# Kernel tuning notes

Hardware: AMD Instinct MI355X
Metric: run time of the kernel (lower is better)

Reference implementation:

```python
import jax, jax.numpy as jnp
import numpy as np

WS = 16            # window size (patch grid)
NP = WS * WS       # 256 patch tokens
N = NP + 1         # +1 CLS
H = 16             # heads
LN_EPS = 1e-5


def _rel_pos_index():
    ch, cw = np.meshgrid(np.arange(WS), np.arange(WS), indexing='ij')
    flat = np.stack([ch.reshape(-1), cw.reshape(-1)])            # [2, NP]
    rel = flat[:, :, None] - flat[:, None, :]                    # [2, NP, NP]
    rel = rel.transpose(1, 2, 0).astype(np.int64)                # [NP, NP, 2]
    rel[:, :, 0] += WS - 1
    rel[:, :, 1] += WS - 1
    rel[:, :, 0] *= 2 * WS - 1
    nrd = (2 * WS - 1) * (2 * WS - 1) + 3                        # 964
    idx = np.zeros((N, N), dtype=np.int64)
    idx[1:, 1:] = rel.sum(-1)
    idx[0, 0:] = nrd - 3
    idx[0:, 0] = nrd - 2
    idx[0, 0] = nrd - 1
    return idx

REL_IDX = _rel_pos_index()


def layernorm(x, g, b):
    mu = x.mean(-1, keepdims=True)
    var = x.var(-1, keepdims=True)
    return (x - mu) * jax.lax.rsqrt(var + LN_EPS) * g + b


def rotate_half(t):
    t1, t2 = t[..., ::2], t[..., 1::2]
    return jnp.stack([-t2, t1], axis=-1).reshape(t.shape)


def apply_rope(t, cos, sin):
    # t: [B, H, NP, hd]; cos/sin: [NP, hd]
    return t * cos + rotate_half(t) * sin


def setup_inputs() -> dict:
    key = jax.random.key(0)
    ks = jax.random.split(key, 20)
    D, Hd = 1024, 4096
    s = lambda d: 1.0 / np.sqrt(d)
    return {
        'x': jax.random.normal(ks[0], (64, N, D), jnp.float32),
        'rope_cos': jnp.cos(jnp.arange(NP)[:, None] * jnp.exp(-jnp.arange(64) / 16.0)[None, :]),
        'rope_sin': jnp.sin(jnp.arange(NP)[:, None] * jnp.exp(-jnp.arange(64) / 16.0)[None, :]),
        'q_w': jax.random.normal(ks[1], (D, D)) * s(D),
        'q_b': jnp.zeros((D,)),
        'k_w': jax.random.normal(ks[2], (D, D)) * s(D),
        'v_w': jax.random.normal(ks[3], (D, D)) * s(D),
        'v_b': jnp.zeros((D,)),
        'rel_bias_table': jax.random.normal(ks[4], (964, H)) * 0.02,
        'inner_ln_g': jnp.ones((D,)), 'inner_ln_b': jnp.zeros((D,)),
        'proj_w': jax.random.normal(ks[5], (D, D)) * s(D),
        'proj_b': jnp.zeros((D,)),
        'norm1_g': jnp.ones((D,)), 'norm1_b': jnp.zeros((D,)),
        'norm2_g': jnp.ones((D,)), 'norm2_b': jnp.zeros((D,)),
        'w1_w': jax.random.normal(ks[6], (Hd, D)) * s(D),
        'w1_b': jnp.zeros((Hd,)),
        'w2_w': jax.random.normal(ks[7], (Hd, D)) * s(D),
        'w2_b': jnp.zeros((Hd,)),
        'ffn_ln_g': jnp.ones((Hd,)), 'ffn_ln_b': jnp.zeros((Hd,)),
        'w3_w': jax.random.normal(ks[8], (D, Hd)) * s(Hd),
        'w3_b': jnp.zeros((D,)),
    }


def reference(x, rope_cos, rope_sin, q_w, q_b, k_w, v_w, v_b, rel_bias_table,
              inner_ln_g, inner_ln_b, proj_w, proj_b, norm1_g, norm1_b,
              norm2_g, norm2_b, w1_w, w1_b, w2_w, w2_b, ffn_ln_g, ffn_ln_b,
              w3_w, w3_b):
    B, Ntok, D = x.shape
    hd = D // H
    scale = hd ** -0.5

    # ---- attention branch (pre-norm, subln path) ----
    xn = layernorm(x, norm1_g, norm1_b)
    q = (xn @ q_w.T + q_b).reshape(B, Ntok, H, hd).transpose(0, 2, 1, 3)
    k = (xn @ k_w.T).reshape(B, Ntok, H, hd).transpose(0, 2, 1, 3)
    v = (xn @ v_w.T + v_b).reshape(B, Ntok, H, hd).transpose(0, 2, 1, 3)

    # RoPE on all tokens except CLS
    q = jnp.concatenate([q[:, :, :1], apply_rope(q[:, :, 1:], rope_cos, rope_sin)], axis=2)
    k = jnp.concatenate([k[:, :, :1], apply_rope(k[:, :, 1:], rope_cos, rope_sin)], axis=2)

    attn = jnp.einsum('bhqd,bhkd->bhqk', q * scale, k)
    # relative position bias: [N, N, H] -> [H, N, N]
    rel_bias = rel_bias_table[REL_IDX.reshape(-1)].reshape(Ntok, Ntok, H).transpose(2, 0, 1)
    attn = attn + rel_bias[None]
    attn = jax.nn.softmax(attn, axis=-1)

    out = jnp.einsum('bhqk,bhkd->bqhd', attn, v).reshape(B, Ntok, D)
    out = layernorm(out, inner_ln_g, inner_ln_b)     # inner_attn_ln (subln)
    out = out @ proj_w.T + proj_b
    x = x + out

    # ---- SwiGLU MLP branch ----
    xn2 = layernorm(x, norm2_g, norm2_b)
    x1 = xn2 @ w1_w.T + w1_b
    x2 = xn2 @ w2_w.T + w2_b
    hidden = jax.nn.silu(x1) * x2
    hidden = layernorm(hidden, ffn_ln_g, ffn_ln_b)   # ffn_ln (subln)
    x = x + (hidden @ w3_w.T + w3_b)
    return x
```

## Files before the change

kernel.cpp:

```cpp
#include <hip/hip_runtime.h>
#include <stdint.h>

typedef __bf16 bf16;
typedef __attribute__((ext_vector_type(8))) __bf16 bf16x8;
typedef __attribute__((ext_vector_type(4))) float floatx4;

__device__ inline float bflo(uint32_t u){ union{uint32_t v; float f;} t; t.v = u << 16; return t.f; }
__device__ inline float bfhi(uint32_t u){ union{uint32_t v; float f;} t; t.v = u & 0xffff0000u; return t.f; }
__device__ inline uint32_t pack2(float a, float b){ union{ bf16 h[2]; uint32_t u; } t; t.h[0]=(bf16)a; t.h[1]=(bf16)b; return t.u; }

__device__ inline void load4(const bf16* p, float* x){
  uint2 u = *(const uint2*)p; x[0]=bflo(u.x); x[1]=bfhi(u.x); x[2]=bflo(u.y); x[3]=bfhi(u.y);
}
__device__ inline void load4(const float* p, float* x){
  float4 u = *(const float4*)p; x[0]=u.x; x[1]=u.y; x[2]=u.z; x[3]=u.w;
}

__device__ inline void gload16(const void* g, void* l){
  __builtin_amdgcn_global_load_lds((const __attribute__((address_space(1))) uint32_t*)g,
                                   (__attribute__((address_space(3))) uint32_t*)l, 16, 0, 0);
}

__global__ __launch_bounds__(256) void cvt_kernel(const float* __restrict__ in, bf16* __restrict__ out,
                                                  int n8, float scale)
{
  int i = blockIdx.x * 256 + threadIdx.x;
  if (i >= n8) return;
  const float* p = in + (size_t)i * 8;
  float4 a = *(const float4*)p;
  float4 b = *(const float4*)(p + 4);
  union{ uint4 q; bf16 h[8]; } pk;
  pk.h[0]=(bf16)(a.x*scale); pk.h[1]=(bf16)(a.y*scale); pk.h[2]=(bf16)(a.z*scale); pk.h[3]=(bf16)(a.w*scale);
  pk.h[4]=(bf16)(b.x*scale); pk.h[5]=(bf16)(b.y*scale); pk.h[6]=(bf16)(b.z*scale); pk.h[7]=(bf16)(b.w*scale);
  *(uint4*)(out + (size_t)i*8) = pk.q;
}

__global__ __launch_bounds__(256) void qkvb_fill(const float* __restrict__ qb, const float* __restrict__ vb,
                                                 float* __restrict__ out)
{
  int i = blockIdx.x * 256 + threadIdx.x;
  float v = 0.f;
  if (i < 1024) v = qb[i] * 0.125f;
  else if (i >= 2048) v = vb[i - 2048];
  out[i] = v;
}

__global__ __launch_bounds__(256) void bias_fill(const float* __restrict__ tab, bf16* __restrict__ biasB)
{
  int t = blockIdx.x * 256 + threadIdx.x;
  if (t >= 16*272*272) return;
  int kg = t % 272;
  int rem = t / 272;
  int qg = rem % 272;
  int h = rem / 272;
  float v;
  if (kg > 256) v = -3e38f;
  else {
    int qq = min(qg, 256);
    int idx;
    if (qq == 0 && kg == 0) idx = 963;
    else if (qq == 0) idx = 961;
    else if (kg == 0) idx = 962;
    else { int p = qq - 1, pk = kg - 1;
           idx = ((p >> 4) - (pk >> 4) + 15) * 31 + ((p & 15) - (pk & 15) + 15); }
    v = tab[idx*16 + h];
  }
  biasB[t] = (bf16)v;
}

template<int W, typename TIN>
__global__ __launch_bounds__(256) void ln_kernel(const TIN* in, const float* __restrict__ g,
                                                 const float* __restrict__ bb, bf16* out, int M)
{
  constexpr int E = W / 256;
  int row = blockIdx.x; if (row >= M) return;
  int tid = threadIdx.x;
  const TIN* rp = in + (size_t)row * W + tid * E;
  float x[E];
  #pragma unroll
  for (int j = 0; j < E; j += 4) load4(rp + j, &x[j]);
  float s = 0.f, ss = 0.f;
  #pragma unroll
  for (int e = 0; e < E; e++){ s += x[e]; ss += x[e]*x[e]; }
  #pragma unroll
  for (int k = 32; k >= 1; k >>= 1){ s += __shfl_xor(s, k, 64); ss += __shfl_xor(ss, k, 64); }
  __shared__ float rs_[4], rq_[4];
  if ((tid & 63) == 0){ rs_[tid >> 6] = s; rq_[tid >> 6] = ss; }
  __syncthreads();
  s = rs_[0]+rs_[1]+rs_[2]+rs_[3]; ss = rq_[0]+rq_[1]+rq_[2]+rq_[3];
  float mean = s * (1.0f / W);
  float var  = ss * (1.0f / W) - mean * mean;
  float rinv = rsqrtf(var + 1e-5f);
  bf16* op = out + (size_t)row * W + tid * E;
  const float* gp = g + tid * E;
  const float* bp = bb + tid * E;
  #pragma unroll
  for (int j = 0; j < E; j += 4){
    float gv[4], bv[4];
    load4(gp + j, gv); load4(bp + j, bv);
    float y0 = (x[j]  -mean)*rinv*gv[0] + bv[0];
    float y1 = (x[j+1]-mean)*rinv*gv[1] + bv[1];
    float y2 = (x[j+2]-mean)*rinv*gv[2] + bv[2];
    float y3 = (x[j+3]-mean)*rinv*gv[3] + bv[3];
    uint2 o; o.x = pack2(y0, y1); o.y = pack2(y2, y3);
    *(uint2*)(op + j) = o;
  }
}

template<typename TE, typename TC>
__global__ __launch_bounds__(256) void gemm_bt(const bf16* __restrict__ A, const bf16* __restrict__ Bw,
                                               const float* __restrict__ bias, const TE* extra,
                                               TC* C, int M, int N, int K, int mode)
{
  __shared__ __align__(16) bf16 As[128*32];
  __shared__ __align__(16) bf16 Bs[128*32];
  int tid = threadIdx.x;
  int lane = tid & 63, wave = tid >> 6;
  int l16 = lane & 15, quad = lane >> 4;
  int wm = wave >> 1, wn = wave & 1;
  int m0 = blockIdx.y * 128, n0 = blockIdx.x * 128;
  floatx4 acc[4][4];
  #pragma unroll
  for (int i = 0; i < 4; i++)
    #pragma unroll
    for (int j = 0; j < 4; j++) acc[i][j] = (floatx4){0.f,0.f,0.f,0.f};
  int nk = K >> 5;
  int rowS = tid >> 2;
  int colS = (tid & 3) * 8;
  int ra0 = min(m0 + rowS,      M-1);
  int ra1 = min(m0 + 64 + rowS, M-1);
  int rb0 = min(n0 + rowS,      N-1);
  int rb1 = min(n0 + 64 + rowS, N-1);
  const bf16* pa0 = A  + (size_t)ra0 * K + colS;
  const bf16* pa1 = A  + (size_t)ra1 * K + colS;
  const bf16* pb0 = Bw + (size_t)rb0 * K + colS;
  const bf16* pb1 = Bw + (size_t)rb1 * K + colS;
  bf16* la0 = &As[tid*8];        bf16* la1 = &As[2048 + tid*8];
  bf16* lb0 = &Bs[tid*8];        bf16* lb1 = &Bs[2048 + tid*8];
  auto stage = [&](int kt){
    int ko = kt * 32;
    gload16(pa0 + ko, la0);
    gload16(pa1 + ko, la1);
    gload16(pb0 + ko, lb0);
    gload16(pb1 + ko, lb1);
  };
  stage(0);
  int kt = 0;
  while (true){
    __syncthreads();
    bf16x8 af[4], bfv[4];
    #pragma unroll
    for (int i = 0; i < 4; i++) af[i]  = *(const bf16x8*)&As[(wm*64 + i*16 + l16)*32 + quad*8];
    #pragma unroll
    for (int j = 0; j < 4; j++) bfv[j] = *(const bf16x8*)&Bs[(wn*64 + j*16 + l16)*32 + quad*8];
    ++kt;
    bool more = kt < nk;
    if (more){
      __syncthreads();
      stage(kt);
    }
    #pragma unroll
    for (int i = 0; i < 4; i++)
      #pragma unroll
      for (int j = 0; j < 4; j++)
        acc[i][j] = __builtin_amdgcn_mfma_f32_16x16x32_bf16(af[i], bfv[j], acc[i][j], 0, 0, 0);
    if (!more) break;
  }
  #pragma unroll
  for (int i = 0; i < 4; i++){
    int gmb = m0 + wm*64 + i*16 + quad*4;
    #pragma unroll
    for (int j = 0; j < 4; j++){
      int gn = n0 + wn*64 + j*16 + l16;
      float bv = bias ? bias[gn] : 0.f;
      #pragma unroll
      for (int r = 0; r < 4; r++){
        int gm = gmb + r;
        if (gm < M){
          float v = acc[i][j][r] + bv;
          if (mode == 1) v += (float)extra[(size_t)gm * N + gn];
          else if (mode == 2){ float a = (float)extra[(size_t)gm * N + gn]; v *= a / (1.f + __expf(-a)); }
          C[(size_t)gm * N + gn] = (TC)v;
        }
      }
    }
  }
}

__global__ __launch_bounds__(256) void rope_kernel(bf16* __restrict__ qkv,
                                                   const float* __restrict__ cs, const float* __restrict__ sn)
{
  uint32_t i = blockIdx.x * 256u + threadIdx.x;
  int d0 = (int)(i & 511) * 2;
  int tok = (int)((i >> 9) & 255);
  int b = (int)(i >> 17);
  int j = d0 & 63;
  float c0 = cs[tok*64 + j], c1 = cs[tok*64 + j + 1];
  float s0 = sn[tok*64 + j], s1 = sn[tok*64 + j + 1];
  size_t off = ((size_t)(b*257 + tok + 1)) * 3072 + d0;
  uint32_t uq = *(const uint32_t*)(qkv + off);
  float x0 = bflo(uq), x1 = bfhi(uq);
  *(uint32_t*)(qkv + off) = pack2(x0*c0 - x1*s0, x1*c1 + x0*s1);
  uint32_t uk = *(const uint32_t*)(qkv + off + 1024);
  float y0 = bflo(uk), y1 = bfhi(uk);
  *(uint32_t*)(qkv + off + 1024) = pack2(y0*c0 - y1*s0, y1*c1 + y0*s1);
}

__global__ __launch_bounds__(256, 2) void attn_kernel(const bf16* __restrict__ QKV,
                                                      const bf16* __restrict__ biasB,
                                                      bf16* __restrict__ AO)
{
  __shared__ __align__(16) bf16 Ks[272*64];
  __shared__ __align__(16) bf16 Vt[64*296];
  int id = blockIdx.x;
  int h = id & 15, b = id >> 4;
  int tid = threadIdx.x, lane = tid & 63, wave = tid >> 6;
  int l16 = lane & 15, quad = lane >> 4;
  size_t baseQ = (size_t)(b*257) * 3072 + h*64;
  const bf16* Kg = QKV + baseQ + 1024;
  const bf16* Vg = QKV + baseQ + 2048;
  size_t aoBase = (size_t)(b*257) * 1024 + h*64;

  for (int i = tid; i < 272*8; i += 256){
    int row = i >> 3, seg = i & 7;
    int tok = min(row, 256);
    gload16(Kg + (size_t)tok*3072 + ((seg ^ (row & 7)) * 8), &Ks[i*8]);
  }
  for (int i = tid; i < 144*8; i += 256){
    int tp = (i % 144) * 2, dseg = i / 144;
    uint4 u0 = make_uint4(0,0,0,0), u1 = make_uint4(0,0,0,0);
    if (tp     <= 256) u0 = *(const uint4*)(Vg + (size_t)tp*3072 + dseg*8);
    if (tp + 1 <= 256) u1 = *(const uint4*)(Vg + (size_t)(tp+1)*3072 + dseg*8);
    union { uint4 q4; bf16 h8[8]; } va, vb2; va.q4 = u0; vb2.q4 = u1;
    #pragma unroll
    for (int jj = 0; jj < 8; jj++){
      union { uint32_t u; bf16 hh[2]; } w; w.hh[0] = va.h8[jj]; w.hh[1] = vb2.h8[jj];
      *(uint32_t*)&Vt[(dseg*8 + jj)*296 + tp] = w.u;
    }
  }
  __syncthreads();

  int srcA = l16 + 16*((2*quad)     & 3);
  int srcB = l16 + 16*((2*quad + 1) & 3);

  for (int qt = wave; qt < 17; qt += 4){
    int q0 = qt * 16;
    int qrow = min(q0 + l16, 256);
    const bf16* qp = QKV + baseQ + (size_t)qrow*3072;
    bf16x8 qb0 = *(const bf16x8*)(qp + quad*8);
    bf16x8 qb1 = *(const bf16x8*)(qp + 32 + quad*8);

    floatx4 S[17];
    #pragma unroll
    for (int nt = 0; nt < 17; nt++){
      int row = nt*16 + l16;
      bf16x8 ka0 = *(const bf16x8*)&Ks[row*64 + ((quad     ^ (l16 & 7)) * 8)];
      bf16x8 ka1 = *(const bf16x8*)&Ks[row*64 + (((4+quad) ^ (l16 & 7)) * 8)];
      floatx4 c = (floatx4){0.f,0.f,0.f,0.f};
      c = __builtin_amdgcn_mfma_f32_16x16x32_bf16(ka0, qb0, c, 0, 0, 0);
      c = __builtin_amdgcn_mfma_f32_16x16x32_bf16(ka1, qb1, c, 0, 0, 0);
      S[nt] = c;
    }

    const bf16* bp = biasB + ((size_t)(h*272) + (q0 + l16)) * 272;
    float m = -3e38f;
    #pragma unroll
    for (int nt = 0; nt < 17; nt++){
      uint2 bu = *(const uint2*)(bp + nt*16 + quad*4);
      S[nt][0] += bflo(bu.x); S[nt][1] += bfhi(bu.x);
      S[nt][2] += bflo(bu.y); S[nt][3] += bfhi(bu.y);
      m = fmaxf(m, fmaxf(fmaxf(S[nt][0], S[nt][1]), fmaxf(S[nt][2], S[nt][3])));
    }
    m = fmaxf(m, __shfl_xor(m, 16, 64));
    m = fmaxf(m, __shfl_xor(m, 32, 64));

    float lsum = 0.f;
    uint32_t pklo[17], pkhi[17];
    #pragma unroll
    for (int nt = 0; nt < 17; nt++){
      float p0 = __expf(S[nt][0] - m), p1 = __expf(S[nt][1] - m);
      float p2 = __expf(S[nt][2] - m), p3 = __expf(S[nt][3] - m);
      lsum += (p0 + p1) + (p2 + p3);
      pklo[nt] = pack2(p0, p1); pkhi[nt] = pack2(p2, p3);
    }
    lsum += __shfl_xor(lsum, 16, 64);
    lsum += __shfl_xor(lsum, 32, 64);

    floatx4 o[4];
    #pragma unroll
    for (int dt = 0; dt < 4; dt++) o[dt] = (floatx4){0.f,0.f,0.f,0.f};
    #pragma unroll
    for (int ks = 0; ks < 9; ks++){
      uint32_t t0[4], t1[4];
      t0[0] = (uint32_t)__shfl((int)pklo[2*ks], srcA, 64);
      t0[1] = (uint32_t)__shfl((int)pkhi[2*ks], srcA, 64);
      t0[2] = (uint32_t)__shfl((int)pklo[2*ks], srcB, 64);
      t0[3] = (uint32_t)__shfl((int)pkhi[2*ks], srcB, 64);
      if (2*ks + 1 <= 16){
        t1[0] = (uint32_t)__shfl((int)pklo[2*ks+1], srcA, 64);
        t1[1] = (uint32_t)__shfl((int)pkhi[2*ks+1], srcA, 64);
        t1[2] = (uint32_t)__shfl((int)pklo[2*ks+1], srcB, 64);
        t1[3] = (uint32_t)__shfl((int)pkhi[2*ks+1], srcB, 64);
      } else {
        t1[0] = 0; t1[1] = 0; t1[2] = 0; t1[3] = 0;
      }
      union { uint32_t u[4]; bf16x8 v; } pa;
      bool lowhalf = (quad < 2);
      pa.u[0] = lowhalf ? t0[0] : t1[0];
      pa.u[1] = lowhalf ? t0[1] : t1[1];
      pa.u[2] = lowhalf ? t0[2] : t1[2];
      pa.u[3] = lowhalf ? t0[3] : t1[3];
      #pragma unroll
      for (int dt = 0; dt < 4; dt++){
        bf16x8 vb = *(const bf16x8*)&Vt[(dt*16 + l16)*296 + ks*32 + quad*8];
        o[dt] = __builtin_amdgcn_mfma_f32_16x16x32_bf16(pa.v, vb, o[dt], 0, 0, 0);
      }
    }

    #pragma unroll
    for (int r = 0; r < 4; r++){
      int q = q0 + quad*4 + r;
      float ls = __shfl(lsum, quad*4 + r, 64);
      float rinv = 1.0f / ls;
      if (q <= 256){
        #pragma unroll
        for (int dt = 0; dt < 4; dt++)
          AO[aoBase + (size_t)q*1024 + dt*16 + l16] = (bf16)(o[dt][r] * rinv);
      }
    }
  }
}

extern "C" void kernel_launch(void* const* d_in, const int* in_sizes, int n_in,
                              void* d_out, int out_size, void* d_ws, size_t ws_size,
                              hipStream_t stream)
{
  (void)in_sizes; (void)n_in; (void)out_size; (void)ws_size;
  const float* x    = (const float*)d_in[0];
  const float* rc   = (const float*)d_in[1];
  const float* rsn  = (const float*)d_in[2];
  const float* q_w  = (const float*)d_in[3];
  const float* q_b  = (const float*)d_in[4];
  const float* k_w  = (const float*)d_in[5];
  const float* v_w  = (const float*)d_in[6];
  const float* v_b  = (const float*)d_in[7];
  const float* tab  = (const float*)d_in[8];
  const float* ig   = (const float*)d_in[9];
  const float* ib   = (const float*)d_in[10];
  const float* pw   = (const float*)d_in[11];
  const float* pb   = (const float*)d_in[12];
  const float* n1g  = (const float*)d_in[13];
  const float* n1b  = (const float*)d_in[14];
  const float* n2g  = (const float*)d_in[15];
  const float* n2b  = (const float*)d_in[16];
  const float* w1w  = (const float*)d_in[17];
  const float* w1b  = (const float*)d_in[18];
  const float* w2w  = (const float*)d_in[19];
  const float* w2b  = (const float*)d_in[20];
  const float* fg   = (const float*)d_in[21];
  const float* fb   = (const float*)d_in[22];
  const float* w3w  = (const float*)d_in[23];
  const float* w3b  = (const float*)d_in[24];

  const int M = 64 * 257;
  const int D = 1024, HD = 4096;
  char* ws = (char*)d_ws;
  const size_t CHB = (size_t)M * D * 2;
  bf16* B0 = (bf16*)(ws);
  bf16* B1 = (bf16*)(ws + CHB);
  bf16* B2 = (bf16*)(ws + 2*CHB);
  bf16* B3 = (bf16*)(ws + 3*CHB);
  bf16* WQ = (bf16*)(ws + 4*CHB);
  bf16* WK = WQ + (size_t)D*D;
  bf16* WV = WK + (size_t)D*D;
  bf16* WP = WV + (size_t)D*D;
  bf16* W1 = WP + (size_t)D*D;
  bf16* W2 = W1 + (size_t)HD*D;
  bf16* W3 = W2 + (size_t)HD*D;
  float* QKVB = (float*)(W3 + (size_t)HD*D);
  bf16* XN  = B0;
  bf16* QKV = B1;
  bf16* AO  = B0;
  bf16* AOL = B1;
  bf16* X1  = B2;
  bf16* XN2 = B3;
  bf16* HS  = B0;
  bf16* biasB = (bf16*)d_out;
  float* OUT = (float*)d_out;

  dim3 blk(256);
  dim3 g1(D/128, (M + 127)/128);
  dim3 gqkv(3072/128, (M + 127)/128);

  const int n8_D = D*D/8;
  const int n8_H = HD*D/8;
  cvt_kernel<<<dim3(n8_D/256), blk, 0, stream>>>(q_w, WQ, n8_D, 0.125f);
  cvt_kernel<<<dim3(n8_D/256), blk, 0, stream>>>(k_w, WK, n8_D, 1.f);
  cvt_kernel<<<dim3(n8_D/256), blk, 0, stream>>>(v_w, WV, n8_D, 1.f);
  cvt_kernel<<<dim3(n8_D/256), blk, 0, stream>>>(pw,  WP, n8_D, 1.f);
  cvt_kernel<<<dim3(n8_H/256), blk, 0, stream>>>(w1w, W1, n8_H, 1.f);
  cvt_kernel<<<dim3(n8_H/256), blk, 0, stream>>>(w2w, W2, n8_H, 1.f);
  cvt_kernel<<<dim3(n8_H/256), blk, 0, stream>>>(w3w, W3, n8_H, 1.f);
  qkvb_fill<<<dim3(12), blk, 0, stream>>>(q_b, v_b, QKVB);
  bias_fill<<<dim3((16*272*272 + 255)/256), blk, 0, stream>>>(tab, biasB);

  ln_kernel<1024, float><<<dim3(M), blk, 0, stream>>>(x, n1g, n1b, XN, M);
  gemm_bt<bf16, bf16><<<gqkv, blk, 0, stream>>>(XN, WQ, QKVB, (const bf16*)nullptr, QKV, M, 3072, D, 0);
  rope_kernel<<<dim3(64*256*512/256), blk, 0, stream>>>(QKV, rc, rsn);
  attn_kernel<<<dim3(64*16), blk, 0, stream>>>(QKV, biasB, AO);
  ln_kernel<1024, bf16><<<dim3(M), blk, 0, stream>>>(AO, ig, ib, AOL, M);
  gemm_bt<float, bf16><<<g1, blk, 0, stream>>>(AOL, WP, pb, x, X1, M, D, D, 1);
  ln_kernel<1024, bf16><<<dim3(M), blk, 0, stream>>>(X1, n2g, n2b, XN2, M);

  const int MC = M / 2;
  dim3 g2(HD/128, (MC + 127)/128);
  dim3 g1c(D/128, (MC + 127)/128);
  for (int c = 0; c < 2; c++){
    const bf16* a2 = XN2 + (size_t)c * MC * D;
    const bf16* x1 = X1  + (size_t)c * MC * D;
    float*      oc = OUT + (size_t)c * MC * D;
    gemm_bt<bf16, bf16><<<g2, blk, 0, stream>>>(a2, W1, w1b, (const bf16*)nullptr, HS, MC, HD, D, 0);
    gemm_bt<bf16, bf16><<<g2, blk, 0, stream>>>(a2, W2, w2b, HS, HS, MC, HD, D, 2);
    ln_kernel<4096, bf16><<<dim3(MC), blk, 0, stream>>>(HS, fg, fb, HS, MC);
    gemm_bt<bf16, float><<<g1c, blk, 0, stream>>>(HS, W3, w3b, x1, oc, MC, D, HD, 1);
  }
}
```

Before: 1.658 ms.

## Coalesce V load, prefetch bias, and stage attention output through LDS

The V tile is now loaded with row-contiguous 16-byte reads, and each row pair is transposed into LDS via lane shuffles, replacing strided per-thread paired-row loads. The LDS row stride drops from 296 to 280. The bias loads are hoisted ahead of the QK MFMAs so their latency overlaps compute. Output is staged through a per-wave LDS buffer so AO stores become 16-byte coalesced writes instead of scattered 2-byte stores. LDS use grows slightly, and the shuffle-based transpose relies on lane pairing, which adds complexity.

```diff
diff --git a/kernel.cpp b/kernel.cpp
--- a/kernel.cpp
+++ b/kernel.cpp
@@ -210,8 +210,10 @@
                                                       const bf16* __restrict__ biasB,
                                                       bf16* __restrict__ AO)
 {
+  constexpr int VS = 280;
   __shared__ __align__(16) bf16 Ks[272*64];
-  __shared__ __align__(16) bf16 Vt[64*296];
+  __shared__ __align__(16) bf16 Vt[64*VS];
+  __shared__ __align__(16) bf16 Os[4][16*72];
   int id = blockIdx.x;
   int h = id & 15, b = id >> 4;
   int tid = threadIdx.x, lane = tid & 63, wave = tid >> 6;
@@ -226,16 +228,29 @@
     int tok = min(row, 256);
     gload16(Kg + (size_t)tok*3072 + ((seg ^ (row & 7)) * 8), &Ks[i*8]);
   }
-  for (int i = tid; i < 144*8; i += 256){
-    int tp = (i % 144) * 2, dseg = i / 144;
-    uint4 u0 = make_uint4(0,0,0,0), u1 = make_uint4(0,0,0,0);
-    if (tp     <= 256) u0 = *(const uint4*)(Vg + (size_t)tp*3072 + dseg*8);
-    if (tp + 1 <= 256) u1 = *(const uint4*)(Vg + (size_t)(tp+1)*3072 + dseg*8);
-    union { uint4 q4; bf16 h8[8]; } va, vb2; va.q4 = u0; vb2.q4 = u1;
-    #pragma unroll
-    for (int jj = 0; jj < 8; jj++){
-      union { uint32_t u; bf16 hh[2]; } w; w.hh[0] = va.h8[jj]; w.hh[1] = vb2.h8[jj];
-      *(uint32_t*)&Vt[(dseg*8 + jj)*296 + tp] = w.u;
+  for (int i = tid; i < 272*8; i += 256){
+    int row = i >> 3, seg = i & 7;
+    int tok = min(row, 256);
+    uint4 v = *(const uint4*)(Vg + (size_t)tok*3072 + seg*8);
+    uint4 w;
+    w.x = (uint32_t)__shfl_xor((int)v.x, 8, 64);
+    w.y = (uint32_t)__shfl_xor((int)v.y, 8, 64);
+    w.z = (uint32_t)__shfl_xor((int)v.z, 8, 64);
+    w.w = (uint32_t)__shfl_xor((int)v.w, 8, 64);
+    union { uint4 q4; bf16 h8[8]; } mv, pv; mv.q4 = v; pv.q4 = w;
+    int rb = row & ~1;
+    if ((row & 1) == 0){
+      #pragma unroll
+      for (int jj = 0; jj < 4; jj++){
+        union { uint32_t u; bf16 hh[2]; } pk; pk.hh[0] = mv.h8[jj]; pk.hh[1] = pv.h8[jj];
+        *(uint32_t*)&Vt[(seg*8 + jj)*VS + rb] = pk.u;
+      }
+    } else {
+      #pragma unroll
+      for (int jj = 4; jj < 8; jj++){
+        union { uint32_t u; bf16 hh[2]; } pk; pk.hh[0] = pv.h8[jj]; pk.hh[1] = mv.h8[jj];
+        *(uint32_t*)&Vt[(seg*8 + jj)*VS + rb] = pk.u;
+      }
     }
   }
   __syncthreads();
@@ -249,6 +264,11 @@
     const bf16* qp = QKV + baseQ + (size_t)qrow*3072;
     bf16x8 qb0 = *(const bf16x8*)(qp + quad*8);
     bf16x8 qb1 = *(const bf16x8*)(qp + 32 + quad*8);
+
+    const bf16* bp = biasB + ((size_t)(h*272) + (q0 + l16)) * 272;
+    uint2 bu[17];
+    #pragma unroll
+    for (int nt = 0; nt < 17; nt++) bu[nt] = *(const uint2*)(bp + nt*16 + quad*4);
 
     floatx4 S[17];
     #pragma unroll
@@ -262,13 +282,11 @@
       S[nt] = c;
     }
 
-    const bf16* bp = biasB + ((size_t)(h*272) + (q0 + l16)) * 272;
     float m = -3e38f;
     #pragma unroll
     for (int nt = 0; nt < 17; nt++){
-      uint2 bu = *(const uint2*)(bp + nt*16 + quad*4);
-      S[nt][0] += bflo(bu.x); S[nt][1] += bfhi(bu.x);
-      S[nt][2] += bflo(bu.y); S[nt][3] += bfhi(bu.y);
+      S[nt][0] += bflo(bu[nt].x); S[nt][1] += bfhi(bu[nt].x);
+      S[nt][2] += bflo(bu[nt].y); S[nt][3] += bfhi(bu[nt].y);
       m = fmaxf(m, fmaxf(fmaxf(S[nt][0], S[nt][1]), fmaxf(S[nt][2], S[nt][3])));
     }
     m = fmaxf(m, __shfl_xor(m, 16, 64));
@@ -312,21 +330,27 @@
       pa.u[3] = lowhalf ? t0[3] : t1[3];
       #pragma unroll
       for (int dt = 0; dt < 4; dt++){
-        bf16x8 vb = *(const bf16x8*)&Vt[(dt*16 + l16)*296 + ks*32 + quad*8];
+        bf16x8 vb = *(const bf16x8*)&Vt[(dt*16 + l16)*VS + ks*32 + quad*8];
         o[dt] = __builtin_amdgcn_mfma_f32_16x16x32_bf16(pa.v, vb, o[dt], 0, 0, 0);
       }
     }
 
     #pragma unroll
     for (int r = 0; r < 4; r++){
-      int q = q0 + quad*4 + r;
-      float ls = __shfl(lsum, quad*4 + r, 64);
+      int qr = quad*4 + r;
+      float ls = __shfl(lsum, qr, 64);
       float rinv = 1.0f / ls;
-      if (q <= 256){
-        #pragma unroll
-        for (int dt = 0; dt < 4; dt++)
-          AO[aoBase + (size_t)q*1024 + dt*16 + l16] = (bf16)(o[dt][r] * rinv);
-      }
+      #pragma unroll
+      for (int dt = 0; dt < 4; dt++)
+        Os[wave][qr*72 + dt*16 + l16] = (bf16)(o[dt][r] * rinv);
+    }
+    #pragma unroll
+    for (int half = 0; half < 2; half++){
+      int rowL = (lane >> 3) + half*8;
+      int chunk = lane & 7;
+      int q = q0 + rowL;
+      uint4 ov = *(const uint4*)&Os[wave][rowL*72 + chunk*8];
+      if (q <= 256) *(uint4*)&AO[aoBase + (size_t)q*1024 + chunk*8] = ov;
     }
   }
 }
```

After: 1.617 ms. 2.5% less time.
